# Performance work log

Hardware: AMD Instinct MI355X
Metric: run time of the kernel (lower is better)

The kernel has to match this reference:

```python
import jax, jax.numpy as jnp
import numpy as np

N, E, F_IN, F_OUT = 8192, 1024, 256, 256


def setup_inputs() -> dict:
    key = jax.random.key(0)
    k1, k2, k3, k4 = jax.random.split(key, 4)
    X = jax.random.normal(k1, (N, F_IN), dtype=jnp.float32)
    # binary incidence matrix: node i belongs to hyperedge j with p=0.05
    H = (jax.random.uniform(k2, (N, E)) < 0.05).astype(jnp.float32)
    W = jax.random.normal(k3, (F_OUT, F_IN), dtype=jnp.float32) * (1.0 / np.sqrt(F_IN))
    b = jax.random.normal(k4, (F_OUT,), dtype=jnp.float32) * 0.01
    return {"X": X, "H": H, "W": W, "b": b}


def reference(X, H, W, b):
    # Dv = diag(row sums of H), De = diag(col sums of H)
    dv = jnp.sum(H, axis=1)                      # [N] node degrees
    de = jnp.sum(H, axis=0)                      # [E] edge degrees
    dv_inv_sqrt = 1.0 / jnp.sqrt(dv)             # inv of sqrt(Dv) (diagonal)
    de_inv = 1.0 / de                            # inv of De (diagonal)
    # diagonal matrices realized as broadcast scalings (same math, no N x N).
    Xs = X * dv_inv_sqrt[:, None]
    M = H.T @ Xs                                 # H^T (...)          [E, F]
    M = M * de_inv[:, None]                      # De^-1 (...)        [E, F]
    X_new = (H @ M) * dv_inv_sqrt[:, None]       # Dv^-1/2 H (...)    [N, F]
    return X_new @ W.T + b                       # nn.Linear
```

## Files before the change

### kernel.cpp

```cpp
#include <hip/hip_runtime.h>
#include <hip/hip_bf16.h>
#include <stdint.h>

typedef __attribute__((ext_vector_type(8))) short bf16x8;
typedef __attribute__((ext_vector_type(4))) float f32x4;
typedef __attribute__((ext_vector_type(4))) unsigned int u32x4;
typedef __attribute__((ext_vector_type(2))) unsigned int u32x2;
typedef unsigned short u16;
typedef unsigned int u32;
typedef unsigned long long u64;

#define N_NODES 8192
#define N_EDGES 1024
#define F_DIM   256
#define NMAX 128
#define NSEG 256

__device__ __forceinline__ u16 f2bf(float f) {
    union { float f; u32 u; } v; v.f = f;
    u32 u = v.u;
    u = (u + 0x7FFFu + ((u >> 16) & 1u)) >> 16;
    return (u16)u;
}
__device__ __forceinline__ float bflo(u32 p) {
    union { u32 u; float f; } v; v.u = p << 16; return v.f;
}
__device__ __forceinline__ float bfhi(u32 p) {
    union { u32 u; float f; } v; v.u = p & 0xffff0000u; return v.f;
}

__global__ __launch_bounds__(512) void prep(
    const float* __restrict__ H, const float* __restrict__ X,
    float* __restrict__ dv, u16* __restrict__ nlist,
    u16* __restrict__ Xs, u32* __restrict__ HbT) {
    __shared__ u16 hmask[32][64];
    const int tid = threadIdx.x;
    const int wv = tid >> 6;
    const int lane = tid & 63;
    const int blk = blockIdx.x;
    const int n0 = blk * 32 + wv * 4;

    f32x4 hv[4][4], xv[4];
#pragma unroll
    for (int r = 0; r < 4; ++r) {
        const int n = n0 + r;
#pragma unroll
        for (int q = 0; q < 4; ++q)
            hv[r][q] = *(const f32x4*)(&H[(size_t)n * N_EDGES + q * 256 + lane * 4]);
        xv[r] = *(const f32x4*)(&X[(size_t)n * F_DIM + lane * 4]);
    }

#pragma unroll
    for (int r = 0; r < 4; ++r) {
        const int n = n0 + r;
        u32 m16 = 0u;
#pragma unroll
        for (int q = 0; q < 4; ++q)
#pragma unroll
            for (int j = 0; j < 4; ++j)
                m16 |= ((hv[r][q][j] != 0.f) ? 1u : 0u) << (q * 4 + j);
        hmask[wv * 4 + r][lane] = (u16)m16;
        const u32 cl = (u32)__popc(m16);
        u32 x = cl;
#pragma unroll
        for (int d = 1; d < 64; d <<= 1) {
            const u32 t = __shfl_up(x, d, 64);
            if (lane >= d) x += t;
        }
        const u32 total = __shfl(x, 63, 64);
        u32 pos = x - cl;
        u16* nrow = &nlist[(size_t)n * NMAX];
        u32 m = m16;
        while (m) {
            const int bidx = __builtin_ctz(m);
            m &= m - 1;
            const int col = ((bidx >> 2) << 8) + lane * 4 + (bidx & 3);
            if (pos < NMAX) nrow[pos] = (u16)col;
            ++pos;
        }
        if (lane == 0) dv[n] = (float)total;
        const float s = rsqrtf((float)total);
        u32x2 pk;
        pk[0] = (u32)f2bf(xv[r][0] * s) | ((u32)f2bf(xv[r][1] * s) << 16);
        pk[1] = (u32)f2bf(xv[r][2] * s) | ((u32)f2bf(xv[r][3] * s) << 16);
        *(u32x2*)(&Xs[(size_t)n * F_DIM + lane * 4]) = pk;
    }
    __syncthreads();
#pragma unroll
    for (int eo = 0; eo < 2; ++eo) {
        const int e = tid + eo * 512;
        const int widx = (e & 255) >> 2;
        const int bit = ((e >> 8) << 2) + (e & 3);
        u32 w = 0u;
#pragma unroll
        for (int r = 0; r < 32; ++r)
            w |= (u32)((hmask[r][widx] >> bit) & 1u) << r;
        HbT[(size_t)e * NSEG + blk] = w;
    }
}

__global__ __launch_bounds__(512) void spmm1(
    const u16* __restrict__ Xs, const u32* __restrict__ HbT,
    u16* __restrict__ Mb) {
    __shared__ u32 words[NSEG];
    __shared__ float red[16][2][128];
    __shared__ u32 wcnt[8];
    const int tid = threadIdx.x;
    const int wv = tid >> 6;
    const int lane = tid & 63;
    const int e = blockIdx.x;
    if (tid < NSEG) words[tid] = HbT[(size_t)e * NSEG + tid];
    __syncthreads();
    const int half = lane >> 5, l32 = lane & 31;
    float a[8] = {};
    u32 cnt = 0;
    for (int s = wv * 32; s < wv * 32 + 32; ++s) {
        u32 w = words[s];
        cnt += (u32)__popc(w);
        const int nb = s * 32;
        while (w) {
            const int b0 = __builtin_ctz(w); w &= w - 1;
            const int b1 = w ? __builtin_ctz(w) : -1;
            if (w) w &= w - 1;
            const int b = half ? b1 : b0;
            if (b >= 0) {
                const int n = nb + b;
                const u32x4 pk = *(const u32x4*)(&Xs[(size_t)n * F_DIM + l32 * 8]);
                a[0] += bflo(pk[0]); a[1] += bfhi(pk[0]);
                a[2] += bflo(pk[1]); a[3] += bfhi(pk[1]);
                a[4] += bflo(pk[2]); a[5] += bfhi(pk[2]);
                a[6] += bflo(pk[3]); a[7] += bfhi(pk[3]);
            }
        }
    }
    const int ws = wv * 2 + half;
    f32x4 r0 = {a[0], a[1], a[2], a[3]};
    f32x4 r1 = {a[4], a[5], a[6], a[7]};
    *(f32x4*)(&red[ws][0][l32 * 4]) = r0;
    *(f32x4*)(&red[ws][1][l32 * 4]) = r1;
    if (lane == 0) wcnt[wv] = cnt;
    __syncthreads();
    if (tid < F_DIM) {
        const int f = tid;
        const int pl = (f >> 2) & 1;
        const int ix = ((f >> 3) << 2) | (f & 3);
        float s = 0.f;
#pragma unroll
        for (int w = 0; w < 16; ++w) s += red[w][pl][ix];
        u32 de = 0;
#pragma unroll
        for (int w = 0; w < 8; ++w) de += wcnt[w];
        Mb[(size_t)e * F_DIM + f] = f2bf(s / (float)de);
    }
}

__global__ __launch_bounds__(256) void gemm_we(
    const u16* __restrict__ Mb, const float* __restrict__ W,
    u16* __restrict__ M2) {
    __shared__ u16 As[64 * 72];
    __shared__ u16 Bs[64 * 72];
    const int tid = threadIdx.x;
    const int lane = tid & 63;
    const int wave = tid >> 6;
    const int wm = wave >> 1, wn = wave & 1;
    const int row16 = lane & 15;
    const int quad = lane >> 4;

    const int e0 = blockIdx.y * 64;
    const int j0 = blockIdx.x * 64;

    const int sr = tid >> 2;
    const int fb = (tid & 3) * 16;

    f32x4 acc[2][2] = {};

    for (int k = 0; k < 256; k += 64) {
        const u32x4 a0 = *(const u32x4*)(&Mb[(size_t)(e0 + sr) * F_DIM + k + fb]);
        const u32x4 a1 = *(const u32x4*)(&Mb[(size_t)(e0 + sr) * F_DIM + k + fb + 8]);
        *(u32x4*)(&As[sr * 72 + fb]) = a0;
        *(u32x4*)(&As[sr * 72 + fb + 8]) = a1;
#pragma unroll
        for (int s2 = 0; s2 < 4; ++s2) {
            f32x4 w = *(const f32x4*)(&W[(size_t)(j0 + sr) * F_DIM + k + fb + s2 * 4]);
            u32x2 pk;
            pk[0] = (u32)f2bf(w[0]) | ((u32)f2bf(w[1]) << 16);
            pk[1] = (u32)f2bf(w[2]) | ((u32)f2bf(w[3]) << 16);
            *(u32x2*)(&Bs[sr * 72 + fb + s2 * 4]) = pk;
        }
        __syncthreads();
#pragma unroll
        for (int ks = 0; ks < 2; ++ks) {
            bf16x8 af[2], bfr[2];
#pragma unroll
            for (int t = 0; t < 2; ++t) {
                af[t]  = *(const bf16x8*)(&As[(wm * 32 + t * 16 + row16) * 72 + ks * 32 + quad * 8]);
                bfr[t] = *(const bf16x8*)(&Bs[(wn * 32 + t * 16 + row16) * 72 + ks * 32 + quad * 8]);
            }
#pragma unroll
            for (int tm = 0; tm < 2; tm++)
#pragma unroll
                for (int tn = 0; tn < 2; tn++)
                    acc[tm][tn] = __builtin_amdgcn_mfma_f32_16x16x32_bf16(
                        af[tm], bfr[tn], acc[tm][tn], 0, 0, 0);
        }
        __syncthreads();
    }

#pragma unroll
    for (int tm = 0; tm < 2; tm++) {
#pragma unroll
        for (int tn = 0; tn < 2; tn++) {
            const int col = j0 + wn * 32 + tn * 16 + row16;
#pragma unroll
            for (int r = 0; r < 4; r++) {
                const int row = e0 + wm * 32 + tm * 16 + quad * 4 + r;
                M2[(size_t)row * F_DIM + col] = f2bf(acc[tm][tn][r]);
            }
        }
    }
}

__global__ __launch_bounds__(256) void spmm2(
    const u16* __restrict__ M2, const float* __restrict__ dv,
    const u16* __restrict__ nlist, const float* __restrict__ bias,
    float* __restrict__ out) {
    __shared__ u16 nl[4 * NMAX];
    __shared__ float red2[4][2][2][128];
    const int tid = threadIdx.x;
    const int wv = tid >> 6, lane = tid & 63;
    const int n = blockIdx.x * 4 + wv;
    if (tid < 256)
        ((u32*)nl)[tid] = ((const u32*)&nlist[(size_t)blockIdx.x * 4 * NMAX])[tid];
    __syncthreads();
    const float dvn = dv[n];
    const int cnt = min((int)dvn, NMAX);
    const u16* lst = &nl[wv * NMAX];
    const int half = lane >> 5;
    const int l32 = lane & 31;
    float a[8] = {};
    const int npairs = (cnt + 1) >> 1;
#pragma unroll 4
    for (int p = 0; p < npairs; ++p) {
        const int idx = 2 * p + half;
        if (idx < cnt) {
            const int e = lst[idx];
            const u32x4 pk = *(const u32x4*)(&M2[(size_t)e * F_DIM + l32 * 8]);
            a[0] += bflo(pk[0]); a[1] += bfhi(pk[0]);
            a[2] += bflo(pk[1]); a[3] += bfhi(pk[1]);
            a[4] += bflo(pk[2]); a[5] += bfhi(pk[2]);
            a[6] += bflo(pk[3]); a[7] += bfhi(pk[3]);
        }
    }
    f32x4 r0 = {a[0], a[1], a[2], a[3]};
    f32x4 r1 = {a[4], a[5], a[6], a[7]};
    *(f32x4*)(&red2[wv][half][0][l32 * 4]) = r0;
    *(f32x4*)(&red2[wv][half][1][l32 * 4]) = r1;
    const float s = rsqrtf(dvn);
    const f32x4 bb = *(const f32x4*)(&bias[lane * 4]);
    const f32x4 v0 = *(const f32x4*)(&red2[wv][0][lane & 1][(lane >> 1) * 4]);
    const f32x4 v1 = *(const f32x4*)(&red2[wv][1][lane & 1][(lane >> 1) * 4]);
    f32x4 r;
#pragma unroll
    for (int k = 0; k < 4; ++k) r[k] = (v0[k] + v1[k]) * s + bb[k];
    *(f32x4*)(&out[(size_t)n * F_DIM + lane * 4]) = r;
}

extern "C" void kernel_launch(void* const* d_in, const int* in_sizes, int n_in,
                              void* d_out, int out_size, void* d_ws, size_t ws_size,
                              hipStream_t stream) {
    (void)in_sizes; (void)n_in; (void)out_size; (void)ws_size;
    const float* X = (const float*)d_in[0];
    const float* H = (const float*)d_in[1];
    const float* W = (const float*)d_in[2];
    const float* b = (const float*)d_in[3];
    float* out = (float*)d_out;

    char* ws = (char*)d_ws;
    float* dv    = (float*)(ws);
    u32*   HbT   = (u32*)(ws + 0x10000);
    u16*   nlist = (u16*)(ws + 0x110000);
    u16*   Xs    = (u16*)(ws + 0x310000);
    u16*   Mb    = (u16*)(ws + 0x710000);
    u16*   M2    = (u16*)(ws + 0x790000);

    prep<<<NSEG, 512, 0, stream>>>(H, X, dv, nlist, Xs, HbT);
    spmm1<<<N_EDGES, 512, 0, stream>>>(Xs, HbT, Mb);
    gemm_we<<<dim3(4, 16), 256, 0, stream>>>(Mb, W, M2);
    spmm2<<<N_NODES / 4, 256, 0, stream>>>(M2, dv, nlist, b, out);
}
```

Measured before the change: 132.3 us.

## Fuse linear projection into node aggregation and compact edge lists in spmm1

Drops the separate gemm_we kernel and the M2 buffer. The node-side gather now runs on un-projected edge features, and each 16-node block then multiplies its rows by W with MFMA, adding the bias. spmm1 also builds a compacted per-edge node list with a wave prefix scan over popcounts and splits it evenly across waves, which removes the bit-scan imbalance between waves. The cost is more GEMM work, since it now covers 8192 rows instead of 1024. W is also reloaded and converted to bf16 from global memory in every block, and edges with more than 512 members are silently truncated.

After: 145.7 us. 1.1x slower.

```diff
diff --git a/kernel.cpp b/kernel.cpp
--- a/kernel.cpp
+++ b/kernel.cpp
@@ -14,6 +14,7 @@
 #define N_EDGES 1024
 #define F_DIM   256
 #define NMAX 128
+#define EMAX 512
 #define NSEG 256
 
 __device__ __forceinline__ u16 f2bf(float f) {
@@ -103,166 +104,159 @@
     const u16* __restrict__ Xs, const u32* __restrict__ HbT,
     u16* __restrict__ Mb) {
     __shared__ u32 words[NSEG];
+    __shared__ u16 lst[EMAX];
+    __shared__ u32 wtot[4];
     __shared__ float red[16][2][128];
-    __shared__ u32 wcnt[8];
     const int tid = threadIdx.x;
     const int wv = tid >> 6;
     const int lane = tid & 63;
     const int e = blockIdx.x;
     if (tid < NSEG) words[tid] = HbT[(size_t)e * NSEG + tid];
     __syncthreads();
+    u32 c = 0, x = 0;
+    if (tid < NSEG) {
+        c = (u32)__popc(words[tid]);
+        x = c;
+#pragma unroll
+        for (int d = 1; d < 64; d <<= 1) {
+            const u32 t = __shfl_up(x, d, 64);
+            if (lane >= d) x += t;
+        }
+        if (lane == 63) wtot[wv] = x;
+    }
+    __syncthreads();
+    if (tid < NSEG) {
+        u32 off = 0;
+        for (int w = 0; w < wv; ++w) off += wtot[w];
+        u32 pos = off + x - c;
+        u32 m = words[tid];
+        const int nb = tid * 32;
+        while (m) {
+            const int b = __builtin_ctz(m);
+            m &= m - 1;
+            if (pos < EMAX) lst[pos] = (u16)(nb + b);
+            ++pos;
+        }
+    }
+    __syncthreads();
+    const u32 de = wtot[0] + wtot[1] + wtot[2] + wtot[3];
+    const int cnt = min((int)de, EMAX);
     const int half = lane >> 5, l32 = lane & 31;
+    const int npairs = (cnt + 1) >> 1;
+    const int len = (npairs + 7) >> 3;
+    const int p0 = wv * len;
+    const int p1 = min(p0 + len, npairs);
     float a[8] = {};
-    u32 cnt = 0;
-    for (int s = wv * 32; s < wv * 32 + 32; ++s) {
-        u32 w = words[s];
-        cnt += (u32)__popc(w);
-        const int nb = s * 32;
-        while (w) {
-            const int b0 = __builtin_ctz(w); w &= w - 1;
-            const int b1 = w ? __builtin_ctz(w) : -1;
-            if (w) w &= w - 1;
-            const int b = half ? b1 : b0;
-            if (b >= 0) {
-                const int n = nb + b;
-                const u32x4 pk = *(const u32x4*)(&Xs[(size_t)n * F_DIM + l32 * 8]);
+#pragma unroll 8
+    for (int p = p0; p < p1; ++p) {
+        const int idx = 2 * p + half;
+        if (idx < cnt) {
+            const int n = lst[idx];
+            const u32x4 pk = *(const u32x4*)(&Xs[(size_t)n * F_DIM + l32 * 8]);
+            a[0] += bflo(pk[0]); a[1] += bfhi(pk[0]);
+            a[2] += bflo(pk[1]); a[3] += bfhi(pk[1]);
+            a[4] += bflo(pk[2]); a[5] += bfhi(pk[2]);
+            a[6] += bflo(pk[3]); a[7] += bfhi(pk[3]);
+        }
+    }
+    const int ws = wv * 2 + half;
+    f32x4 r0 = {a[0], a[1], a[2], a[3]};
+    f32x4 r1 = {a[4], a[5], a[6], a[7]};
+    *(f32x4*)(&red[ws][0][l32 * 4]) = r0;
+    *(f32x4*)(&red[ws][1][l32 * 4]) = r1;
+    __syncthreads();
+    if (tid < F_DIM) {
+        const int f = tid;
+        const int pl = (f >> 2) & 1;
+        const int ix = ((f >> 3) << 2) | (f & 3);
+        float s = 0.f;
+#pragma unroll
+        for (int w = 0; w < 16; ++w) s += red[w][pl][ix];
+        Mb[(size_t)e * F_DIM + f] = f2bf(s / (float)de);
+    }
+}
+
+__global__ __launch_bounds__(256) void spmm2w(
+    const u16* __restrict__ Mb, const float* __restrict__ dv,
+    const u16* __restrict__ nlist, const float* __restrict__ W,
+    const float* __restrict__ bias, float* __restrict__ out) {
+    __shared__ u16 nl[16 * NMAX];
+    __shared__ u16 Yb[16][264];
+    __shared__ float redA[4][2][256];
+    const int tid = threadIdx.x;
+    const int wv = tid >> 6;
+    const int lane = tid & 63;
+    const int n0 = blockIdx.x * 16;
+    {
+        const u32* gn = (const u32*)&nlist[(size_t)n0 * NMAX];
+#pragma unroll
+        for (int k = 0; k < 4; ++k)
+            ((u32*)nl)[tid + k * 256] = gn[tid + k * 256];
+    }
+    __syncthreads();
+    const int half = lane >> 5, l32 = lane & 31;
+#pragma unroll
+    for (int r = 0; r < 4; ++r) {
+        const int row = wv * 4 + r;
+        const int n = n0 + row;
+        const float dvn = dv[n];
+        const int cnt = min((int)dvn, NMAX);
+        const u16* lt = &nl[row * NMAX];
+        float a[8] = {};
+        const int npairs = (cnt + 1) >> 1;
+#pragma unroll 8
+        for (int p = 0; p < npairs; ++p) {
+            const int idx = 2 * p + half;
+            if (idx < cnt) {
+                const int e = lt[idx];
+                const u32x4 pk = *(const u32x4*)(&Mb[(size_t)e * F_DIM + l32 * 8]);
                 a[0] += bflo(pk[0]); a[1] += bfhi(pk[0]);
                 a[2] += bflo(pk[1]); a[3] += bfhi(pk[1]);
                 a[4] += bflo(pk[2]); a[5] += bfhi(pk[2]);
                 a[6] += bflo(pk[3]); a[7] += bfhi(pk[3]);
             }
         }
-    }
-    const int ws = wv * 2 + half;
-    f32x4 r0 = {a[0], a[1], a[2], a[3]};
-    f32x4 r1 = {a[4], a[5], a[6], a[7]};
-    *(f32x4*)(&red[ws][0][l32 * 4]) = r0;
-    *(f32x4*)(&red[ws][1][l32 * 4]) = r1;
-    if (lane == 0) wcnt[wv] = cnt;
-    __syncthreads();
-    if (tid < F_DIM) {
-        const int f = tid;
-        const int pl = (f >> 2) & 1;
-        const int ix = ((f >> 3) << 2) | (f & 3);
-        float s = 0.f;
-#pragma unroll
-        for (int w = 0; w < 16; ++w) s += red[w][pl][ix];
-        u32 de = 0;
-#pragma unroll
-        for (int w = 0; w < 8; ++w) de += wcnt[w];
-        Mb[(size_t)e * F_DIM + f] = f2bf(s / (float)de);
-    }
-}
-
-__global__ __launch_bounds__(256) void gemm_we(
-    const u16* __restrict__ Mb, const float* __restrict__ W,
-    u16* __restrict__ M2) {
-    __shared__ u16 As[64 * 72];
-    __shared__ u16 Bs[64 * 72];
-    const int tid = threadIdx.x;
-    const int lane = tid & 63;
-    const int wave = tid >> 6;
-    const int wm = wave >> 1, wn = wave & 1;
-    const int row16 = lane & 15;
-    const int quad = lane >> 4;
-
-    const int e0 = blockIdx.y * 64;
-    const int j0 = blockIdx.x * 64;
-
-    const int sr = tid >> 2;
-    const int fb = (tid & 3) * 16;
-
-    f32x4 acc[2][2] = {};
-
-    for (int k = 0; k < 256; k += 64) {
-        const u32x4 a0 = *(const u32x4*)(&Mb[(size_t)(e0 + sr) * F_DIM + k + fb]);
-        const u32x4 a1 = *(const u32x4*)(&Mb[(size_t)(e0 + sr) * F_DIM + k + fb + 8]);
-        *(u32x4*)(&As[sr * 72 + fb]) = a0;
-        *(u32x4*)(&As[sr * 72 + fb + 8]) = a1;
-#pragma unroll
-        for (int s2 = 0; s2 < 4; ++s2) {
-            f32x4 w = *(const f32x4*)(&W[(size_t)(j0 + sr) * F_DIM + k + fb + s2 * 4]);
-            u32x2 pk;
-            pk[0] = (u32)f2bf(w[0]) | ((u32)f2bf(w[1]) << 16);
-            pk[1] = (u32)f2bf(w[2]) | ((u32)f2bf(w[3]) << 16);
-            *(u32x2*)(&Bs[sr * 72 + fb + s2 * 4]) = pk;
-        }
-        __syncthreads();
-#pragma unroll
-        for (int ks = 0; ks < 2; ++ks) {
-            bf16x8 af[2], bfr[2];
-#pragma unroll
-            for (int t = 0; t < 2; ++t) {
-                af[t]  = *(const bf16x8*)(&As[(wm * 32 + t * 16 + row16) * 72 + ks * 32 + quad * 8]);
-                bfr[t] = *(const bf16x8*)(&Bs[(wn * 32 + t * 16 + row16) * 72 + ks * 32 + quad * 8]);
-            }
-#pragma unroll
-            for (int tm = 0; tm < 2; tm++)
-#pragma unroll
-                for (int tn = 0; tn < 2; tn++)
-                    acc[tm][tn] = __builtin_amdgcn_mfma_f32_16x16x32_bf16(
-                        af[tm], bfr[tn], acc[tm][tn], 0, 0, 0);
-        }
-        __syncthreads();
-    }
-
-#pragma unroll
-    for (int tm = 0; tm < 2; tm++) {
-#pragma unroll
-        for (int tn = 0; tn < 2; tn++) {
-            const int col = j0 + wn * 32 + tn * 16 + row16;
-#pragma unroll
-            for (int r = 0; r < 4; r++) {
-                const int row = e0 + wm * 32 + tm * 16 + quad * 4 + r;
-                M2[(size_t)row * F_DIM + col] = f2bf(acc[tm][tn][r]);
-            }
-        }
-    }
-}
-
-__global__ __launch_bounds__(256) void spmm2(
-    const u16* __restrict__ M2, const float* __restrict__ dv,
-    const u16* __restrict__ nlist, const float* __restrict__ bias,
-    float* __restrict__ out) {
-    __shared__ u16 nl[4 * NMAX];
-    __shared__ float red2[4][2][2][128];
-    const int tid = threadIdx.x;
-    const int wv = tid >> 6, lane = tid & 63;
-    const int n = blockIdx.x * 4 + wv;
-    if (tid < 256)
-        ((u32*)nl)[tid] = ((const u32*)&nlist[(size_t)blockIdx.x * 4 * NMAX])[tid];
-    __syncthreads();
-    const float dvn = dv[n];
-    const int cnt = min((int)dvn, NMAX);
-    const u16* lst = &nl[wv * NMAX];
-    const int half = lane >> 5;
-    const int l32 = lane & 31;
-    float a[8] = {};
-    const int npairs = (cnt + 1) >> 1;
-#pragma unroll 4
-    for (int p = 0; p < npairs; ++p) {
-        const int idx = 2 * p + half;
-        if (idx < cnt) {
-            const int e = lst[idx];
-            const u32x4 pk = *(const u32x4*)(&M2[(size_t)e * F_DIM + l32 * 8]);
-            a[0] += bflo(pk[0]); a[1] += bfhi(pk[0]);
-            a[2] += bflo(pk[1]); a[3] += bfhi(pk[1]);
-            a[4] += bflo(pk[2]); a[5] += bfhi(pk[2]);
-            a[6] += bflo(pk[3]); a[7] += bfhi(pk[3]);
-        }
-    }
-    f32x4 r0 = {a[0], a[1], a[2], a[3]};
-    f32x4 r1 = {a[4], a[5], a[6], a[7]};
-    *(f32x4*)(&red2[wv][half][0][l32 * 4]) = r0;
-    *(f32x4*)(&red2[wv][half][1][l32 * 4]) = r1;
-    const float s = rsqrtf(dvn);
-    const f32x4 bb = *(const f32x4*)(&bias[lane * 4]);
-    const f32x4 v0 = *(const f32x4*)(&red2[wv][0][lane & 1][(lane >> 1) * 4]);
-    const f32x4 v1 = *(const f32x4*)(&red2[wv][1][lane & 1][(lane >> 1) * 4]);
-    f32x4 r;
-#pragma unroll
-    for (int k = 0; k < 4; ++k) r[k] = (v0[k] + v1[k]) * s + bb[k];
-    *(f32x4*)(&out[(size_t)n * F_DIM + lane * 4]) = r;
+        f32x4 v0 = {a[0], a[1], a[2], a[3]};
+        f32x4 v1 = {a[4], a[5], a[6], a[7]};
+        *(f32x4*)(&redA[wv][half][l32 * 8]) = v0;
+        *(f32x4*)(&redA[wv][half][l32 * 8 + 4]) = v1;
+        const float s = rsqrtf(dvn);
+        const f32x4 u0 = *(const f32x4*)(&redA[wv][0][lane * 4]);
+        const f32x4 u1 = *(const f32x4*)(&redA[wv][1][lane * 4]);
+        u32x2 pk;
+        pk[0] = (u32)f2bf((u0[0] + u1[0]) * s) | ((u32)f2bf((u0[1] + u1[1]) * s) << 16);
+        pk[1] = (u32)f2bf((u0[2] + u1[2]) * s) | ((u32)f2bf((u0[3] + u1[3]) * s) << 16);
+        *(u32x2*)(&Yb[row][lane * 4]) = pk;
+    }
+    __syncthreads();
+    const int row16 = lane & 15, quad = lane >> 4;
+    const int jbase = wv * 64;
+    f32x4 acc[4] = {};
+    for (int ko = 0; ko < 256; ko += 32) {
+        const bf16x8 af = *(const bf16x8*)(&Yb[row16][ko + quad * 8]);
+#pragma unroll
+        for (int tn = 0; tn < 4; ++tn) {
+            const int j = jbase + tn * 16 + row16;
+            const f32x4 w0 = *(const f32x4*)(&W[(size_t)j * F_DIM + ko + quad * 8]);
+            const f32x4 w1 = *(const f32x4*)(&W[(size_t)j * F_DIM + ko + quad * 8 + 4]);
+            union { u32x4 u; bf16x8 b; } bf;
+            bf.u[0] = (u32)f2bf(w0[0]) | ((u32)f2bf(w0[1]) << 16);
+            bf.u[1] = (u32)f2bf(w0[2]) | ((u32)f2bf(w0[3]) << 16);
+            bf.u[2] = (u32)f2bf(w1[0]) | ((u32)f2bf(w1[1]) << 16);
+            bf.u[3] = (u32)f2bf(w1[2]) | ((u32)f2bf(w1[3]) << 16);
+            acc[tn] = __builtin_amdgcn_mfma_f32_16x16x32_bf16(af, bf.b, acc[tn], 0, 0, 0);
+        }
+    }
+#pragma unroll
+    for (int tn = 0; tn < 4; ++tn) {
+        const int col = jbase + tn * 16 + row16;
+        const float bc = bias[col];
+#pragma unroll
+        for (int r2 = 0; r2 < 4; ++r2) {
+            const int n = n0 + quad * 4 + r2;
+            out[(size_t)n * F_DIM + col] = acc[tn][r2] + bc;
+        }
+    }
 }
 
 extern "C" void kernel_launch(void* const* d_in, const int* in_sizes, int n_in,
@@ -281,10 +275,8 @@
     u16*   nlist = (u16*)(ws + 0x110000);
     u16*   Xs    = (u16*)(ws + 0x310000);
     u16*   Mb    = (u16*)(ws + 0x710000);
-    u16*   M2    = (u16*)(ws + 0x790000);
 
     prep<<<NSEG, 512, 0, stream>>>(H, X, dv, nlist, Xs, HbT);
     spmm1<<<N_EDGES, 512, 0, stream>>>(Xs, HbT, Mb);
-    gemm_we<<<dim3(4, 16), 256, 0, stream>>>(Mb, W, M2);
-    spmm2<<<N_NODES / 4, 256, 0, stream>>>(M2, dv, nlist, b, out);
-}
+    spmm2w<<<N_NODES / 16, 256, 0, stream>>>(Mb, dv, nlist, W, b, out);
+}
```
